# Optimization experiments

Measured on AMD Instinct MI355X. Metric: run time of the kernel, lower is better.

## Reference

```python
import jax, jax.numpy as jnp
import numpy as np

# kernel / loss hyperparameters (from base_params)
FIT_SIGMA = 1.0
FIT_L = 1.0
MMD_SIGMA = 1.0
MMD_L = 2.0
REG_LAMBDA = 0.01

N, D = 8192, 16


def setup_inputs() -> dict:
    key = jax.random.key(0)
    k1, k2, k3 = jax.random.split(key, 3)
    X = jax.random.normal(k1, (N, D), dtype=jnp.float32)
    Y = jax.random.normal(k2, (N, D), dtype=jnp.float32)
    Lam = jax.random.normal(k3, (N, D), dtype=jnp.float32)  # nn.init.normal_ on zeros(N,d)
    return {"X": X, "Y": Y, "Lam": Lam}


def _rbf_gram(X, sigma, l):
    # k(xi, xj) = sigma^2 * exp(-||xi - xj||^2 / (2 l^2)), vectorized over all pairs
    sq = jnp.sum(X * X, axis=1)                      # [N]
    d2 = sq[:, None] + sq[None, :] - 2.0 * (X @ X.T)  # [N, N] squared distances
    d2 = jnp.maximum(d2, 0.0)
    return (sigma ** 2) * jnp.exp(-d2 / (2.0 * l ** 2))


def reference(X, Y, Lam):
    fit_kXX = _rbf_gram(X, FIT_SIGMA, FIT_L)   # [N, N]
    mmd_kXX = _rbf_gram(X, MMD_SIGMA, MMD_L)   # [N, N]
    diff = fit_kXX @ Lam - Y                   # [N, d]
    # trace(diff^T K diff) = sum(diff * (K @ diff))
    loss_fit = jnp.sum(diff * (mmd_kXX @ diff))
    loss_reg = REG_LAMBDA * jnp.sum(Lam * (fit_kXX @ Lam))
    return loss_fit + loss_reg
```

## Files before the change

kernel.cpp:

```cpp
#include <hip/hip_runtime.h>

#define NPTS 8192
#define DIM  16

constexpr int BLK = 256;
constexpr int NIB = NPTS / BLK;

#define REG_LAMBDA 0.01f
#define C1 1.2011224087864498f
#define C2 0.6005612043932249f

typedef _Float16 h4 __attribute__((ext_vector_type(4)));
typedef float    f4 __attribute__((ext_vector_type(4)));

#define MFMA16(a, b, c) __builtin_amdgcn_mfma_f32_16x16x16f16((a), (b), (c), 0, 0, 0)

#if __has_builtin(__builtin_amdgcn_exp2f)
#define EXP2(x) __builtin_amdgcn_exp2f(x)
#else
#define EXP2(x) exp2f(x)
#endif

__device__ __forceinline__ float dot4(float4 a, float4 b) {
  return fmaf(a.x, b.x, fmaf(a.y, b.y, fmaf(a.z, b.z, a.w * b.w)));
}
__device__ __forceinline__ void add4(float4& a, float4 b) {
  a.x += b.x; a.y += b.y; a.z += b.z; a.w += b.w;
}

__device__ __forceinline__ float block_sum(float v, float* wbuf) {
#pragma unroll
  for (int o = 32; o > 0; o >>= 1) v += __shfl_down(v, o, 64);
  const int lane = threadIdx.x & 63;
  const int wid  = threadIdx.x >> 6;
  __syncthreads();
  if (lane == 0) wbuf[wid] = v;
  __syncthreads();
  float s = 0.f;
  if (threadIdx.x == 0) {
#pragma unroll
    for (int w = 0; w < BLK / 64; ++w) s += wbuf[w];
  }
  return s;
}

__global__ __launch_bounds__(BLK) void k_prep(
    const float4* __restrict__ Xv, const float4* __restrict__ Lv,
    _Float16* __restrict__ Xh1, _Float16* __restrict__ Xh2,
    _Float16* __restrict__ LamT,
    float* __restrict__ csq1, float* __restrict__ csq2) {
  const int i = blockIdx.x * BLK + threadIdx.x;
  float sq1 = 0.f, sq2 = 0.f;
  h4* x1 = (h4*)(Xh1 + (size_t)i * DIM);
  h4* x2 = (h4*)(Xh2 + (size_t)i * DIM);
#pragma unroll
  for (int q = 0; q < 4; ++q) {
    const float4 v = Xv[(size_t)i * 4 + q];
    h4 a = {(_Float16)(C1 * v.x), (_Float16)(C1 * v.y),
            (_Float16)(C1 * v.z), (_Float16)(C1 * v.w)};
    h4 b = {(_Float16)(C2 * v.x), (_Float16)(C2 * v.y),
            (_Float16)(C2 * v.z), (_Float16)(C2 * v.w)};
    x1[q] = a; x2[q] = b;
#pragma unroll
    for (int t = 0; t < 4; ++t) {
      const float fa = (float)a[t], fb = (float)b[t];
      sq1 = fmaf(fa, fa, sq1);
      sq2 = fmaf(fb, fb, sq2);
    }
    const float4 l = Lv[(size_t)i * 4 + q];
    LamT[(size_t)(4 * q + 0) * NPTS + i] = (_Float16)l.x;
    LamT[(size_t)(4 * q + 1) * NPTS + i] = (_Float16)l.y;
    LamT[(size_t)(4 * q + 2) * NPTS + i] = (_Float16)l.z;
    LamT[(size_t)(4 * q + 3) * NPTS + i] = (_Float16)l.w;
  }
  csq1[i] = -0.5f * sq1;
  csq2[i] = -0.5f * sq2;
}

__global__ __launch_bounds__(BLK) void k_pass1(
    const _Float16* __restrict__ Xh1, const _Float16* __restrict__ LamT,
    const float* __restrict__ csq1, float* __restrict__ Upart, int span) {
  const int lane = threadIdx.x & 63;
  const int w    = threadIdx.x >> 6;
  const int l16  = lane & 15;
  const int quad = lane >> 4;

  const int i0 = blockIdx.x * 128 + w * 32;
  const h4 bxi0 = *(const h4*)(Xh1 + (size_t)(i0 + l16) * DIM + quad * 4);
  const h4 bxi1 = *(const h4*)(Xh1 + (size_t)(i0 + 16 + l16) * DIM + quad * 4);
  const float ci0 = csq1[i0 + l16];
  const float ci1 = csq1[i0 + 16 + l16];
  const _Float16* blrow = LamT + (size_t)l16 * NPTS;

  f4 U0 = {0.f, 0.f, 0.f, 0.f}, U1 = U0;
  const int jbeg = blockIdx.y * span;
  const int jend = jbeg + span;
#pragma unroll 2
  for (int j0 = jbeg; j0 < jend; j0 += 16) {
    const h4 axj = *(const h4*)(Xh1 + (size_t)(j0 + l16) * DIM + quad * 4);
    const float4 cjf = *(const float4*)(csq1 + j0 + quad * 4);
    const f4 cc0 = {cjf.x + ci0, cjf.y + ci0, cjf.z + ci0, cjf.w + ci0};
    const f4 cc1 = {cjf.x + ci1, cjf.y + ci1, cjf.z + ci1, cjf.w + ci1};
    const f4 p0 = MFMA16(axj, bxi0, cc0);
    const f4 p1 = MFMA16(axj, bxi1, cc1);
    h4 ap0, ap1;
#pragma unroll
    for (int r = 0; r < 4; ++r) {
      ap0[r] = (_Float16)EXP2(p0[r]);
      ap1[r] = (_Float16)EXP2(p1[r]);
    }
    const h4 bl = *(const h4*)(blrow + j0 + quad * 4);
    U0 = MFMA16(ap0, bl, U0);
    U1 = MFMA16(ap1, bl, U1);
  }

  float* dst = Upart + ((size_t)blockIdx.y * NPTS + i0) * DIM;
#pragma unroll
  for (int r = 0; r < 4; ++r) {
    dst[(quad * 4 + r) * DIM + l16]        = U0[r];
    dst[(16 + quad * 4 + r) * DIM + l16]   = U1[r];
  }
}

__global__ __launch_bounds__(BLK) void k_reduce(
    const float4* __restrict__ Upart, const float4* __restrict__ Yv,
    const float4* __restrict__ Lv, _Float16* __restrict__ Dh,
    float* __restrict__ accums, int jc) {
  __shared__ float wred[BLK / 64];
  const int t = blockIdx.x * BLK + threadIdx.x;
  const int i = t >> 2, q = t & 3;
  float4 u = {0.f, 0.f, 0.f, 0.f};
  for (int c = 0; c < jc; ++c)
    add4(u, Upart[((size_t)c * NPTS + i) * 4 + q]);
  const float4 y = Yv[(size_t)i * 4 + q];
  h4 d = {(_Float16)(u.x - y.x), (_Float16)(u.y - y.y),
          (_Float16)(u.z - y.z), (_Float16)(u.w - y.w)};
  *(h4*)(Dh + (size_t)i * DIM + q * 4) = d;
  const float regp = dot4(Lv[(size_t)i * 4 + q], u);
  const float rtot = block_sum(regp, wred);
  if (threadIdx.x == 0) unsafeAtomicAdd(&accums[1], rtot);
}

__global__ __launch_bounds__(BLK) void k_pass2(
    const _Float16* __restrict__ Xh2, const _Float16* __restrict__ Dh,
    const float* __restrict__ csq2, float* __restrict__ accums, int span) {
  __shared__ float wred[BLK / 64];
  const int lane = threadIdx.x & 63;
  const int w    = threadIdx.x >> 6;
  const int l16  = lane & 15;
  const int quad = lane >> 4;
  const f4 fz = {0.f, 0.f, 0.f, 0.f};

  const int i0 = blockIdx.x * 128 + w * 32;
  const h4 ax0 = *(const h4*)(Xh2 + (size_t)(i0 + l16) * DIM + quad * 4);
  const h4 ax1 = *(const h4*)(Xh2 + (size_t)(i0 + 16 + l16) * DIM + quad * 4);
  const h4 ad0 = *(const h4*)(Dh  + (size_t)(i0 + l16) * DIM + quad * 4);
  const h4 ad1 = *(const h4*)(Dh  + (size_t)(i0 + 16 + l16) * DIM + quad * 4);
  const float4 cif0 = *(const float4*)(csq2 + i0 + quad * 4);
  const float4 cif1 = *(const float4*)(csq2 + i0 + 16 + quad * 4);

  float s = 0.f;
  const int jbeg = blockIdx.y * span;
  const int jend = jbeg + span;
#pragma unroll 2
  for (int j0 = jbeg; j0 < jend; j0 += 16) {
    const h4 bx = *(const h4*)(Xh2 + (size_t)(j0 + l16) * DIM + quad * 4);
    const h4 bd = *(const h4*)(Dh  + (size_t)(j0 + l16) * DIM + quad * 4);
    const float cj = csq2[j0 + l16];
    const f4 cc0 = {cif0.x + cj, cif0.y + cj, cif0.z + cj, cif0.w + cj};
    const f4 cc1 = {cif1.x + cj, cif1.y + cj, cif1.z + cj, cif1.w + cj};
    const f4 dx0 = MFMA16(ax0, bx, cc0);
    const f4 dd0 = MFMA16(ad0, bd, fz);
    const f4 dx1 = MFMA16(ax1, bx, cc1);
    const f4 dd1 = MFMA16(ad1, bd, fz);
#pragma unroll
    for (int r = 0; r < 4; ++r) {
      s = fmaf(EXP2(dx0[r]), dd0[r], s);
      s = fmaf(EXP2(dx1[r]), dd1[r], s);
    }
  }

  const float stot = block_sum(s, wred);
  if (threadIdx.x == 0) unsafeAtomicAdd(&accums[0], stot);
}

__global__ void k_final(const float* __restrict__ accums, float* __restrict__ out) {
  out[0] = accums[0] + REG_LAMBDA * accums[1];
}

extern "C" void kernel_launch(void* const* d_in, const int* in_sizes, int n_in,
                              void* d_out, int out_size, void* d_ws, size_t ws_size,
                              hipStream_t stream) {
  const float4* Xv = (const float4*)d_in[0];
  const float4* Yv = (const float4*)d_in[1];
  const float4* Lv = (const float4*)d_in[2];
  float* out = (float*)d_out;

  char* base = (char*)d_ws;
  _Float16* Xh1  = (_Float16*)(base);
  _Float16* Xh2  = (_Float16*)(base + 256 * 1024);
  _Float16* LamT = (_Float16*)(base + 512 * 1024);
  _Float16* Dh   = (_Float16*)(base + 768 * 1024);
  float*    csq1 = (float*)(base + 1024 * 1024);
  float*    csq2 = (float*)(base + 1056 * 1024);
  float*    accums = (float*)(base + 1088 * 1024);
  float*    Upart  = (float*)(base + 1088 * 1024 + 256);
  const size_t fixed = 1088 * 1024 + 256;

  int jc = 16;
  while (jc > 1 && fixed + (size_t)jc * NPTS * DIM * 4 > ws_size) jc >>= 1;
  const int span1 = NPTS / jc;
  const int jc2 = 16, span2 = NPTS / jc2;

  hipMemsetAsync(accums, 0, 2 * sizeof(float), stream);
  k_prep<<<NIB, BLK, 0, stream>>>(Xv, Lv, Xh1, Xh2, LamT, csq1, csq2);
  k_pass1<<<dim3(NPTS / 128, jc), BLK, 0, stream>>>(Xh1, LamT, csq1, Upart, span1);
  k_reduce<<<NPTS * 4 / BLK, BLK, 0, stream>>>((const float4*)Upart, Yv, Lv, Dh, accums, jc);
  k_pass2<<<dim3(NPTS / 128, jc2), BLK, 0, stream>>>(Xh2, Dh, csq2, accums, span2);
  k_final<<<1, 1, 0, stream>>>(accums, out);
}
```

Before: 120.6 us.

## Exploit kernel symmetry in pass2, fold accumulator reset into prep

Pass2 now evaluates only the upper-triangular block pairs of the symmetric MMD quadratic form. Off-diagonal 256x256 tiles are weighted by two and the diagonal band once, which roughly halves the exp and MFMA work. Each wave now handles 64 rows instead of 32, the memset launch is dropped by zeroing the accumulators inside k_prep, and pass1 uses a larger j-split (32 chunks) with the Lam load hoisted earlier. The cost is more Upart partials to reduce in k_reduce and higher register pressure per wave in pass2.

After: 122.8 us. Within noise of the previous version (+1.9%).

```diff
diff --git a/kernel.cpp b/kernel.cpp
--- a/kernel.cpp
+++ b/kernel.cpp
@@ -48,7 +48,11 @@
     const float4* __restrict__ Xv, const float4* __restrict__ Lv,
     _Float16* __restrict__ Xh1, _Float16* __restrict__ Xh2,
     _Float16* __restrict__ LamT,
-    float* __restrict__ csq1, float* __restrict__ csq2) {
+    float* __restrict__ csq1, float* __restrict__ csq2,
+    float* __restrict__ accums) {
+  if (blockIdx.x == 0 && threadIdx.x == 0) {
+    accums[0] = 0.f; accums[1] = 0.f;
+  }
   const int i = blockIdx.x * BLK + threadIdx.x;
   float sq1 = 0.f, sq2 = 0.f;
   h4* x1 = (h4*)(Xh1 + (size_t)i * DIM);
@@ -99,6 +103,7 @@
   for (int j0 = jbeg; j0 < jend; j0 += 16) {
     const h4 axj = *(const h4*)(Xh1 + (size_t)(j0 + l16) * DIM + quad * 4);
     const float4 cjf = *(const float4*)(csq1 + j0 + quad * 4);
+    const h4 bl = *(const h4*)(blrow + j0 + quad * 4);
     const f4 cc0 = {cjf.x + ci0, cjf.y + ci0, cjf.z + ci0, cjf.w + ci0};
     const f4 cc1 = {cjf.x + ci1, cjf.y + ci1, cjf.z + ci1, cjf.w + ci1};
     const f4 p0 = MFMA16(axj, bxi0, cc0);
@@ -109,7 +114,6 @@
       ap0[r] = (_Float16)EXP2(p0[r]);
       ap1[r] = (_Float16)EXP2(p1[r]);
     }
-    const h4 bl = *(const h4*)(blrow + j0 + quad * 4);
     U0 = MFMA16(ap0, bl, U0);
     U1 = MFMA16(ap1, bl, U1);
   }
@@ -117,8 +121,8 @@
   float* dst = Upart + ((size_t)blockIdx.y * NPTS + i0) * DIM;
 #pragma unroll
   for (int r = 0; r < 4; ++r) {
-    dst[(quad * 4 + r) * DIM + l16]        = U0[r];
-    dst[(16 + quad * 4 + r) * DIM + l16]   = U1[r];
+    dst[(quad * 4 + r) * DIM + l16]      = U0[r];
+    dst[(16 + quad * 4 + r) * DIM + l16] = U1[r];
   }
 }
 
@@ -143,44 +147,50 @@
 
 __global__ __launch_bounds__(BLK) void k_pass2(
     const _Float16* __restrict__ Xh2, const _Float16* __restrict__ Dh,
-    const float* __restrict__ csq2, float* __restrict__ accums, int span) {
+    const float* __restrict__ csq2, float* __restrict__ accums) {
   __shared__ float wred[BLK / 64];
+  const int bi   = blockIdx.x;
+  const int k    = blockIdx.y >> 1;
+  const int half = blockIdx.y & 1;
+  if (k == 16 && bi >= 16) return;
+  const int bj = (bi + k) & 31;
+  const float weight = (k == 0) ? 1.f : 2.f;
+
   const int lane = threadIdx.x & 63;
   const int w    = threadIdx.x >> 6;
   const int l16  = lane & 15;
   const int quad = lane >> 4;
   const f4 fz = {0.f, 0.f, 0.f, 0.f};
 
-  const int i0 = blockIdx.x * 128 + w * 32;
-  const h4 ax0 = *(const h4*)(Xh2 + (size_t)(i0 + l16) * DIM + quad * 4);
-  const h4 ax1 = *(const h4*)(Xh2 + (size_t)(i0 + 16 + l16) * DIM + quad * 4);
-  const h4 ad0 = *(const h4*)(Dh  + (size_t)(i0 + l16) * DIM + quad * 4);
-  const h4 ad1 = *(const h4*)(Dh  + (size_t)(i0 + 16 + l16) * DIM + quad * 4);
-  const float4 cif0 = *(const float4*)(csq2 + i0 + quad * 4);
-  const float4 cif1 = *(const float4*)(csq2 + i0 + 16 + quad * 4);
+  const int i0 = bi * 256 + w * 64;
+  h4 ax[4], ad[4];
+  float4 cif[4];
+#pragma unroll
+  for (int t = 0; t < 4; ++t) {
+    ax[t] = *(const h4*)(Xh2 + (size_t)(i0 + 16 * t + l16) * DIM + quad * 4);
+    ad[t] = *(const h4*)(Dh  + (size_t)(i0 + 16 * t + l16) * DIM + quad * 4);
+    cif[t] = *(const float4*)(csq2 + i0 + 16 * t + quad * 4);
+  }
 
   float s = 0.f;
-  const int jbeg = blockIdx.y * span;
-  const int jend = jbeg + span;
+  const int jbeg = bj * 256 + half * 128;
+  const int jend = jbeg + 128;
 #pragma unroll 2
   for (int j0 = jbeg; j0 < jend; j0 += 16) {
     const h4 bx = *(const h4*)(Xh2 + (size_t)(j0 + l16) * DIM + quad * 4);
     const h4 bd = *(const h4*)(Dh  + (size_t)(j0 + l16) * DIM + quad * 4);
     const float cj = csq2[j0 + l16];
-    const f4 cc0 = {cif0.x + cj, cif0.y + cj, cif0.z + cj, cif0.w + cj};
-    const f4 cc1 = {cif1.x + cj, cif1.y + cj, cif1.z + cj, cif1.w + cj};
-    const f4 dx0 = MFMA16(ax0, bx, cc0);
-    const f4 dd0 = MFMA16(ad0, bd, fz);
-    const f4 dx1 = MFMA16(ax1, bx, cc1);
-    const f4 dd1 = MFMA16(ad1, bd, fz);
-#pragma unroll
-    for (int r = 0; r < 4; ++r) {
-      s = fmaf(EXP2(dx0[r]), dd0[r], s);
-      s = fmaf(EXP2(dx1[r]), dd1[r], s);
+#pragma unroll
+    for (int t = 0; t < 4; ++t) {
+      const f4 cc = {cif[t].x + cj, cif[t].y + cj, cif[t].z + cj, cif[t].w + cj};
+      const f4 dx = MFMA16(ax[t], bx, cc);
+      const f4 dd = MFMA16(ad[t], bd, fz);
+#pragma unroll
+      for (int r = 0; r < 4; ++r) s = fmaf(EXP2(dx[r]), dd[r], s);
     }
   }
 
-  const float stot = block_sum(s, wred);
+  const float stot = block_sum(s * weight, wred);
   if (threadIdx.x == 0) unsafeAtomicAdd(&accums[0], stot);
 }
 
@@ -207,15 +217,13 @@
   float*    Upart  = (float*)(base + 1088 * 1024 + 256);
   const size_t fixed = 1088 * 1024 + 256;
 
-  int jc = 16;
+  int jc = 32;
   while (jc > 1 && fixed + (size_t)jc * NPTS * DIM * 4 > ws_size) jc >>= 1;
   const int span1 = NPTS / jc;
-  const int jc2 = 16, span2 = NPTS / jc2;
-
-  hipMemsetAsync(accums, 0, 2 * sizeof(float), stream);
-  k_prep<<<NIB, BLK, 0, stream>>>(Xv, Lv, Xh1, Xh2, LamT, csq1, csq2);
+
+  k_prep<<<NIB, BLK, 0, stream>>>(Xv, Lv, Xh1, Xh2, LamT, csq1, csq2, accums);
   k_pass1<<<dim3(NPTS / 128, jc), BLK, 0, stream>>>(Xh1, LamT, csq1, Upart, span1);
   k_reduce<<<NPTS * 4 / BLK, BLK, 0, stream>>>((const float4*)Upart, Yv, Lv, Dh, accums, jc);
-  k_pass2<<<dim3(NPTS / 128, jc2), BLK, 0, stream>>>(Xh2, Dh, csq2, accums, span2);
+  k_pass2<<<dim3(32, 34), BLK, 0, stream>>>(Xh2, Dh, csq2, accums);
   k_final<<<1, 1, 0, stream>>>(accums, out);
 }
```
